# Kernel optimization log

Hardware: AMD Instinct MI355X
Metric: run time of the kernel (lower is better)

The kernel has to match this reference:

```python
import jax, jax.numpy as jnp
import numpy as np

B, L, D, H = 16, 1024, 1024, 16
HD = D // H  # head dim = 64


def setup_inputs() -> dict:
    rng = jax.random.key(0)
    ks = jax.random.split(rng, 12)
    s = 0.02
    return {
        "key": jax.random.normal(ks[0], (B, L, D), jnp.float32),
        "value": jax.random.normal(ks[1], (B, L, D), jnp.float32),
        "query": jax.random.normal(ks[2], (B, L, D), jnp.float32),
        "atten_masks": jax.random.randint(ks[3], (B, L, L), 0, 2, jnp.int32),
        "Wk": jax.random.normal(ks[4], (D, D), jnp.float32) * s,
        "bk": jnp.zeros((D,), jnp.float32),
        "Wq": jax.random.normal(ks[5], (D, D), jnp.float32) * s,
        "bq": jnp.zeros((D,), jnp.float32),
        "Wv": jax.random.normal(ks[6], (D, D), jnp.float32) * s,
        "bv": jnp.zeros((D,), jnp.float32),
        "Wp": jax.random.normal(ks[7], (D, D), jnp.float32) * s,
        "bp": jnp.zeros((D,), jnp.float32),
    }


def reference(key, value, query, atten_masks, Wk, bk, Wq, bq, Wv, bv, Wp, bp):
    # Linear projections (torch nn.Linear: x @ W^T + b)
    def lin(x, W, b):
        return x @ W.T + b

    # [B, L, D] -> [B, H, L, HD]
    def heads(x):
        return x.reshape(B, L, H, HD).transpose(0, 2, 1, 3)

    k = heads(lin(key, Wk, bk))
    q = heads(lin(query, Wq, bq))
    v = heads(lin(value, Wv, bv))

    scale = 1.0 / np.sqrt(HD).astype(np.float32)
    att = jnp.einsum("bhqd,bhkd->bhqk", q, k) * scale  # [B, H, L, L]
    att = jnp.where(atten_masks[:, None, :, :] == 0, -jnp.inf, att)
    att = jax.nn.softmax(att, axis=-1)

    y = jnp.einsum("bhqk,bhkd->bhqd", att, v)  # [B, H, L, HD]
    y = y.transpose(0, 2, 1, 3).reshape(B, L, D)
    return lin(y, Wp, bp)
```

## Files before the change

kernel.cpp:

```cpp
#include <hip/hip_runtime.h>

typedef __bf16 bf16_t;
typedef __bf16 bf16x4 __attribute__((ext_vector_type(4)));
typedef __bf16 bf16x8 __attribute__((ext_vector_type(8)));
typedef float f32x4 __attribute__((ext_vector_type(4)));
typedef float f32x16 __attribute__((ext_vector_type(16)));
typedef unsigned u32x2 __attribute__((ext_vector_type(2)));

__device__ __forceinline__ int swz(int row) { return (row ^ (row >> 3)) & 7; }
__device__ __forceinline__ int swz2(int row) { return (row ^ (row >> 2)) & 3; }

__device__ __forceinline__ f32x4 mfma16(bf16x8 a, bf16x8 b, f32x4 c) {
  return __builtin_amdgcn_mfma_f32_16x16x32_bf16(a, b, c, 0, 0, 0);
}
__device__ __forceinline__ f32x16 mfma32(bf16x8 a, bf16x8 b, f32x16 c) {
  return __builtin_amdgcn_mfma_f32_32x32x16_bf16(a, b, c, 0, 0, 0);
}

__device__ __forceinline__ void gl_lds16(const void* g, void* l) {
  __builtin_amdgcn_global_load_lds(
      (const __attribute__((address_space(1))) unsigned int*)g,
      (__attribute__((address_space(3))) unsigned int*)l, 16, 0, 0);
}

__global__ __launch_bounds__(256) void cvt_all_kernel(
    const float* __restrict__ key, const float* __restrict__ query,
    const float* __restrict__ value, const float* __restrict__ Wk,
    const float* __restrict__ Wq, const float* __restrict__ Wv,
    const float* __restrict__ Wp, const int* __restrict__ mask,
    bf16_t* __restrict__ I1, bf16_t* __restrict__ I2, bf16_t* __restrict__ I3,
    bf16_t* __restrict__ Wkb, bf16_t* __restrict__ Wqb,
    bf16_t* __restrict__ Wvb, bf16_t* __restrict__ Wpb,
    unsigned* __restrict__ mbits) {
  const int bid = blockIdx.x;
  if (bid >= 53248) {
    int idx = (bid - 53248) * 256 + threadIdx.x;
    const int4* src = (const int4*)(mask + (size_t)idx * 32);
    unsigned w = 0;
#pragma unroll
    for (int i = 0; i < 8; ++i) {
      int4 v = src[i];
      w |= (v.x != 0 ? 1u : 0u) << (i * 4 + 0);
      w |= (v.y != 0 ? 1u : 0u) << (i * 4 + 1);
      w |= (v.z != 0 ? 1u : 0u) << (i * 4 + 2);
      w |= (v.w != 0 ? 1u : 0u) << (i * 4 + 3);
    }
    mbits[idx] = w;
    return;
  }
  const float* s;
  bf16_t* d;
  int base;
  if (bid < 16384) { s = key; d = I1; base = bid; }
  else if (bid < 32768) { s = query; d = I2; base = bid - 16384; }
  else if (bid < 49152) { s = value; d = I3; base = bid - 32768; }
  else if (bid < 50176) { s = Wk; d = Wkb; base = bid - 49152; }
  else if (bid < 51200) { s = Wq; d = Wqb; base = bid - 50176; }
  else if (bid < 52224) { s = Wv; d = Wvb; base = bid - 51200; }
  else { s = Wp; d = Wpb; base = bid - 52224; }
  int i = base * 256 + threadIdx.x;
  float4 v = ((const float4*)s)[i];
  bf16x4 o;
  o[0] = (bf16_t)v.x; o[1] = (bf16_t)v.y; o[2] = (bf16_t)v.z; o[3] = (bf16_t)v.w;
  ((bf16x4*)d)[i] = o;
}

template <typename OT>
__device__ __forceinline__ void gemm256_body(const bf16_t* __restrict__ A,
                                             const bf16_t* __restrict__ W,
                                             const float* __restrict__ bias,
                                             OT* __restrict__ O) {
  extern __shared__ __align__(16) char smem[];
  bf16_t* AsBase = (bf16_t*)smem;
  bf16_t* BsBase = (bf16_t*)(smem + 3 * 8192 * 2);

  const int t = threadIdx.x;
  const int lane = t & 63;
  const int wid = t >> 6;
  const int g = lane >> 4;
  const int lr = lane & 15;
  const int wm = wid >> 2, wn = wid & 3;
  const int lid = blockIdx.x;
  const int logical = (lid & 7) * 32 + (lid >> 3);
  const int m0 = (logical >> 2) * 256;
  const int n0 = (logical & 3) * 256;

  f32x4 acc[8][4] = {};

  auto STAGE = [&](int buf, int kb) {
    bf16_t* Ab = AsBase + buf * 8192;
    bf16_t* Bb = BsBase + buf * 8192;
#pragma unroll
    for (int rr = 0; rr < 2; ++rr) {
      int s = rr * 512 + t;
      int row = s >> 2, c = s & 3;
      gl_lds16(A + (size_t)(m0 + row) * 1024 + kb + (c ^ swz2(row)) * 8,
               &Ab[(rr * 512 + wid * 64) * 8]);
      gl_lds16(W + (size_t)(n0 + row) * 1024 + kb + (c ^ swz2(row)) * 8,
               &Bb[(rr * 512 + wid * 64) * 8]);
    }
  };

  STAGE(0, 0);
  STAGE(1, 32);

  int cur = 0;
  for (int kb = 0; kb < 1024; kb += 32) {
    if (kb + 32 < 1024)
      asm volatile("s_waitcnt vmcnt(4)" ::: "memory");
    else
      asm volatile("s_waitcnt vmcnt(0)" ::: "memory");
    __builtin_amdgcn_sched_barrier(0);
    __builtin_amdgcn_s_barrier();
    __builtin_amdgcn_sched_barrier(0);

    if (kb + 64 < 1024) {
      int fut = cur + 2;
      if (fut >= 3) fut -= 3;
      STAGE(fut, kb + 64);
    }

    const bf16_t* Ab = AsBase + cur * 8192;
    const bf16_t* Bb = BsBase + cur * 8192;
    bf16x8 a[8], b[4];
#pragma unroll
    for (int i = 0; i < 8; ++i) {
      int row = wm * 128 + i * 16 + lr;
      a[i] = *(const bf16x8*)&Ab[row * 32 + ((g ^ swz2(row))) * 8];
    }
#pragma unroll
    for (int j = 0; j < 4; ++j) {
      int row = wn * 64 + j * 16 + lr;
      b[j] = *(const bf16x8*)&Bb[row * 32 + ((g ^ swz2(row))) * 8];
    }
    __builtin_amdgcn_s_setprio(1);
#pragma unroll
    for (int i = 0; i < 8; ++i)
#pragma unroll
      for (int j = 0; j < 4; ++j)
        acc[i][j] = mfma16(a[i], b[j], acc[i][j]);
    __builtin_amdgcn_s_setprio(0);

    cur = (cur == 2) ? 0 : cur + 1;
  }

  float bval[4];
#pragma unroll
  for (int j = 0; j < 4; ++j) bval[j] = bias[n0 + wn * 64 + j * 16 + lr];
#pragma unroll
  for (int i = 0; i < 8; ++i)
#pragma unroll
    for (int r = 0; r < 4; ++r) {
      int row = m0 + wm * 128 + i * 16 + g * 4 + r;
#pragma unroll
      for (int j = 0; j < 4; ++j) {
        int n = n0 + wn * 64 + j * 16 + lr;
        O[(size_t)row * 1024 + n] = (OT)(acc[i][j][r] + bval[j]);
      }
    }
}

__global__ __launch_bounds__(512, 2) void gemm256_qkv_kernel(
    const bf16_t* key, const bf16_t* query, const bf16_t* value,
    const bf16_t* Wkb, const bf16_t* Wqb, const bf16_t* Wvb, const float* bk,
    const float* bq, const float* bv, bf16_t* ko, bf16_t* qo, bf16_t* vo) {
  const bf16_t *A, *W;
  const float* bi;
  bf16_t* O;
  if (blockIdx.y == 0) { A = key; W = Wkb; bi = bk; O = ko; }
  else if (blockIdx.y == 1) { A = query; W = Wqb; bi = bq; O = qo; }
  else { A = value; W = Wvb; bi = bv; O = vo; }
  gemm256_body<bf16_t>(A, W, bi, O);
}

__global__ __launch_bounds__(512, 2) void gemm256_out_kernel(
    const bf16_t* __restrict__ A, const bf16_t* __restrict__ W,
    const float* __restrict__ b, float* __restrict__ O) {
  gemm256_body<float>(A, W, b, O);
}

__global__ __launch_bounds__(256) void transpose_v_kernel(
    const bf16_t* __restrict__ v_ws, bf16_t* __restrict__ vT) {
  __shared__ bf16_t T[64 * 66];
  const int kc = blockIdx.x, h = blockIdx.y, b = blockIdx.z;
  const int t = threadIdx.x;
  {
    int key = t >> 2, dblk = t & 3;
    const bf16_t* src =
        v_ws + ((size_t)(b * 1024 + kc * 64 + key)) * 1024 + h * 64 + dblk * 16;
    bf16x8 a0 = *(const bf16x8*)src;
    bf16x8 a1 = *(const bf16x8*)(src + 8);
    bf16_t* row = &T[key * 66 + dblk * 16];
#pragma unroll
    for (int j = 0; j < 4; ++j) {
      ((unsigned*)row)[j] = ((const unsigned*)&a0)[j];
      ((unsigned*)row)[j + 4] = ((const unsigned*)&a1)[j];
    }
  }
  __syncthreads();
  {
    int d = t >> 2, kcl = t & 3;
    bf16x8 o0, o1;
#pragma unroll
    for (int e = 0; e < 8; ++e) {
      o0[e] = T[(kcl * 16 + e) * 66 + d];
      o1[e] = T[(kcl * 16 + 8 + e) * 66 + d];
    }
    bf16_t* dst =
        vT + ((size_t)((b * 16 + h) * 64 + d)) * 1024 + kc * 64 + kcl * 16;
    *(bf16x8*)dst = o0;
    *(bf16x8*)(dst + 8) = o1;
  }
}

__global__ __launch_bounds__(256) void attn_kernel(
    const bf16_t* __restrict__ q_ws, const bf16_t* __restrict__ k_ws,
    const bf16_t* __restrict__ vT, const unsigned* __restrict__ mbits,
    bf16_t* __restrict__ y_ws) {
  __shared__ __align__(16) bf16_t Ks[64 * 64];
  __shared__ __align__(16) bf16_t Vs[64 * 64];

  const int lid = blockIdx.x;
  const int logical = (lid & 7) * 256 + (lid >> 3);
  const int qb = logical & 7;
  const int h = (logical >> 3) & 15;
  const int b = logical >> 7;
  const int t = threadIdx.x, lane = t & 63, wid = t >> 6;
  const int ql = lane & 31;
  const int hh = lane >> 5;
  const int q = qb * 128 + wid * 32 + ql;

  bf16x8 qf[4];
  {
    const bf16_t* qp = q_ws + ((size_t)(b * 1024 + q)) * 1024 + h * 64 + hh * 8;
#pragma unroll
    for (int kc = 0; kc < 4; ++kc) {
      bf16x8 raw = *(const bf16x8*)(qp + kc * 16);
      bf16x8 sc;
#pragma unroll
      for (int e = 0; e < 8; ++e)
        sc[e] = (bf16_t)((float)raw[e] * 0.18033688f);
      qf[kc] = sc;
    }
  }

  bf16x8 onesf;
#pragma unroll
  for (int e = 0; e < 8; ++e) onesf[e] = (bf16_t)1.0f;

  f32x16 acc0 = {}, acc1 = {}, accl = {};
  const bf16_t* Kb = k_ws + ((size_t)b * 1024) * 1024 + h * 64;
  const bf16_t* Vb = vT + ((size_t)((b * 16 + h) * 64)) * 1024;
  const unsigned* mrow = mbits + ((size_t)(b * 1024 + q)) * 32;

  for (int kb = 0; kb < 16; ++kb) {
    __syncthreads();
#pragma unroll
    for (int rr = 0; rr < 2; ++rr) {
      int s = rr * 256 + t;
      int row = s >> 3, c = s & 7;
      gl_lds16(Kb + (size_t)(kb * 64 + row) * 1024 + (c ^ swz(row)) * 8,
               &Ks[(rr * 256 + wid * 64) * 8]);
      gl_lds16(Vb + (size_t)row * 1024 + kb * 64 + (c ^ swz(row)) * 8,
               &Vs[(rr * 256 + wid * 64) * 8]);
    }
    uint2 mw = *(const uint2*)&mrow[kb * 2];
    __syncthreads();

    f32x16 c0 = {}, c1 = {};
    __builtin_amdgcn_s_setprio(1);
#pragma unroll
    for (int kc = 0; kc < 4; ++kc) {
      int sl = kc * 2 + hh;
      {
        int row = ql;
        bf16x8 kf = *(const bf16x8*)&Ks[row * 64 + ((sl ^ swz(row))) * 8];
        c0 = mfma32(kf, qf[kc], c0);
      }
      {
        int row = 32 + ql;
        bf16x8 kf = *(const bf16x8*)&Ks[row * 64 + ((sl ^ swz(row))) * 8];
        c1 = mfma32(kf, qf[kc], c1);
      }
    }
    __builtin_amdgcn_s_setprio(0);

    unsigned wx = mw.x >> (4 * hh);
    unsigned wy = mw.y >> (4 * hh);
    float p0[16], p1[16];
#pragma unroll
    for (int r = 0; r < 16; ++r) {
      const int posr = (r & 3) + 8 * (r >> 2);
      int n0m = (int)(wx << (31 - posr)) >> 31;
      int n1m = (int)(wy << (31 - posr)) >> 31;
      float e0 = __builtin_amdgcn_exp2f(c0[r]);
      float e1 = __builtin_amdgcn_exp2f(c1[r]);
      p0[r] = __int_as_float(__float_as_int(e0) & n0m);
      p1[r] = __int_as_float(__float_as_int(e1) & n1m);
    }

    bf16x8 pb[4];
#pragma unroll
    for (int kc = 0; kc < 4; ++kc) {
      const int base = (kc & 1) * 8;
      unsigned lo0, lo1, hi0, hi1;
      if (kc < 2) {
        union { bf16_t h[2]; unsigned u; } a0, a1, b0, b1;
        a0.h[0] = (bf16_t)p0[base + 0]; a0.h[1] = (bf16_t)p0[base + 1];
        a1.h[0] = (bf16_t)p0[base + 2]; a1.h[1] = (bf16_t)p0[base + 3];
        b0.h[0] = (bf16_t)p0[base + 4]; b0.h[1] = (bf16_t)p0[base + 5];
        b1.h[0] = (bf16_t)p0[base + 6]; b1.h[1] = (bf16_t)p0[base + 7];
        lo0 = a0.u; lo1 = a1.u; hi0 = b0.u; hi1 = b1.u;
      } else {
        union { bf16_t h[2]; unsigned u; } a0, a1, b0, b1;
        a0.h[0] = (bf16_t)p1[base + 0]; a0.h[1] = (bf16_t)p1[base + 1];
        a1.h[0] = (bf16_t)p1[base + 2]; a1.h[1] = (bf16_t)p1[base + 3];
        b0.h[0] = (bf16_t)p1[base + 4]; b0.h[1] = (bf16_t)p1[base + 5];
        b1.h[0] = (bf16_t)p1[base + 6]; b1.h[1] = (bf16_t)p1[base + 7];
        lo0 = a0.u; lo1 = a1.u; hi0 = b0.u; hi1 = b1.u;
      }
      u32x2 s0 = __builtin_amdgcn_permlane32_swap(lo0, hi0, false, false);
      u32x2 s1 = __builtin_amdgcn_permlane32_swap(lo1, hi1, false, false);
      union { unsigned u[4]; bf16x8 v; } pk;
      pk.u[0] = s0.x;
      pk.u[1] = s1.x;
      pk.u[2] = s0.y;
      pk.u[3] = s1.y;
      pb[kc] = pk.v;
    }

    __builtin_amdgcn_s_setprio(1);
#pragma unroll
    for (int kc = 0; kc < 4; ++kc) {
      int sl = kc * 2 + hh;
      {
        int row = ql;
        bf16x8 vf = *(const bf16x8*)&Vs[row * 64 + ((sl ^ swz(row))) * 8];
        acc0 = mfma32(vf, pb[kc], acc0);
      }
      {
        int row = 32 + ql;
        bf16x8 vf = *(const bf16x8*)&Vs[row * 64 + ((sl ^ swz(row))) * 8];
        acc1 = mfma32(vf, pb[kc], acc1);
      }
      accl = mfma32(onesf, pb[kc], accl);
    }
    __builtin_amdgcn_s_setprio(0);
  }

  float inv = 1.0f / fmaxf(accl[0], 1e-30f);
  bf16_t* yp = y_ws + ((size_t)(b * 1024 + q)) * 1024 + h * 64;
#pragma unroll
  for (int j = 0; j < 4; ++j) {
    bf16x4 o0, o1;
#pragma unroll
    for (int e = 0; e < 4; ++e) {
      o0[e] = (bf16_t)(acc0[4 * j + e] * inv);
      o1[e] = (bf16_t)(acc1[4 * j + e] * inv);
    }
    *(bf16x4*)&yp[8 * j + 4 * hh] = o0;
    *(bf16x4*)&yp[32 + 8 * j + 4 * hh] = o1;
  }
}

extern "C" void kernel_launch(void* const* d_in, const int* in_sizes, int n_in,
                              void* d_out, int out_size, void* d_ws,
                              size_t ws_size, hipStream_t stream) {
  (void)in_sizes; (void)n_in; (void)out_size; (void)ws_size;
  const float* key = (const float*)d_in[0];
  const float* value = (const float*)d_in[1];
  const float* query = (const float*)d_in[2];
  const int* mask = (const int*)d_in[3];
  const float* Wk = (const float*)d_in[4];
  const float* bk = (const float*)d_in[5];
  const float* Wq = (const float*)d_in[6];
  const float* bq = (const float*)d_in[7];
  const float* Wv = (const float*)d_in[8];
  const float* bv = (const float*)d_in[9];
  const float* Wp = (const float*)d_in[10];
  const float* bp = (const float*)d_in[11];
  float* out = (float*)d_out;

  char* ws = (char*)d_ws;
  const size_t MB = 1ull << 20;
  unsigned* mbits = (unsigned*)(ws);
  bf16_t* Wkb = (bf16_t*)(ws + 2 * MB);
  bf16_t* Wqb = (bf16_t*)(ws + 4 * MB);
  bf16_t* Wvb = (bf16_t*)(ws + 6 * MB);
  bf16_t* Wpb = (bf16_t*)(ws + 8 * MB);
  bf16_t* I1 = (bf16_t*)(ws + 10 * MB);
  bf16_t* I2 = (bf16_t*)(ws + 42 * MB);
  bf16_t* I3 = (bf16_t*)(ws + 74 * MB);
  bf16_t* k_ws = (bf16_t*)(ws + 106 * MB);
  bf16_t* q_ws = (bf16_t*)(ws + 138 * MB);
  bf16_t* v_ws = (bf16_t*)(ws + 170 * MB);
  bf16_t* vT_ws = I1;
  bf16_t* y_ws = I2;

  const size_t GEMM_LDS = 3 * 8192 * 2 * 2;

  cvt_all_kernel<<<55296, 256, 0, stream>>>(key, query, value, Wk, Wq, Wv, Wp,
                                            mask, I1, I2, I3, Wkb, Wqb, Wvb,
                                            Wpb, mbits);
  gemm256_qkv_kernel<<<dim3(256, 3), 512, GEMM_LDS, stream>>>(
      I1, I2, I3, Wkb, Wqb, Wvb, bk, bq, bv, k_ws, q_ws, v_ws);
  transpose_v_kernel<<<dim3(16, 16, 16), 256, 0, stream>>>(v_ws, vT_ws);
  attn_kernel<<<2048, 256, 0, stream>>>(q_ws, k_ws, vT_ws, mbits, y_ws);
  gemm256_out_kernel<<<256, 512, GEMM_LDS, stream>>>(y_ws, Wpb, bp, out);
}
```

Before: 355.2 us.

## Triple-buffer K/V tiles in attention and fold query scale into Wq

The attention kernel now keeps three LDS buffers for K and V tiles and prefetches tile kb+2 with global_load_lds while computing tile kb. This replaces the two barriers per iteration with a single barrier plus a manual vmcnt wait. The query scale factor, which includes log2e for exp2, moves from the attention kernel into the Wq conversion and the q bias. This saves per-element conversion work in attention at the cost of scaling Wq before its bf16 rounding, which changes rounding slightly. The hard-coded vmcnt(5) count depends on exactly how many vector memory ops are in flight, which is fragile.

Result: no change. 360.1 us (+1.4%).

```diff
diff --git a/kernel.cpp b/kernel.cpp
--- a/kernel.cpp
+++ b/kernel.cpp
@@ -6,6 +6,8 @@
 typedef float f32x4 __attribute__((ext_vector_type(4)));
 typedef float f32x16 __attribute__((ext_vector_type(16)));
 typedef unsigned u32x2 __attribute__((ext_vector_type(2)));
+
+#define QSCALE 0.18033688f
 
 __device__ __forceinline__ int swz(int row) { return (row ^ (row >> 3)) & 7; }
 __device__ __forceinline__ int swz2(int row) { return (row ^ (row >> 2)) & 3; }
@@ -51,17 +53,19 @@
   const float* s;
   bf16_t* d;
   int base;
+  float sc = 1.0f;
   if (bid < 16384) { s = key; d = I1; base = bid; }
   else if (bid < 32768) { s = query; d = I2; base = bid - 16384; }
   else if (bid < 49152) { s = value; d = I3; base = bid - 32768; }
   else if (bid < 50176) { s = Wk; d = Wkb; base = bid - 49152; }
-  else if (bid < 51200) { s = Wq; d = Wqb; base = bid - 50176; }
+  else if (bid < 51200) { s = Wq; d = Wqb; base = bid - 50176; sc = QSCALE; }
   else if (bid < 52224) { s = Wv; d = Wvb; base = bid - 51200; }
   else { s = Wp; d = Wpb; base = bid - 52224; }
   int i = base * 256 + threadIdx.x;
   float4 v = ((const float4*)s)[i];
   bf16x4 o;
-  o[0] = (bf16_t)v.x; o[1] = (bf16_t)v.y; o[2] = (bf16_t)v.z; o[3] = (bf16_t)v.w;
+  o[0] = (bf16_t)(v.x * sc); o[1] = (bf16_t)(v.y * sc);
+  o[2] = (bf16_t)(v.z * sc); o[3] = (bf16_t)(v.w * sc);
   ((bf16x4*)d)[i] = o;
 }
 
@@ -69,6 +73,7 @@
 __device__ __forceinline__ void gemm256_body(const bf16_t* __restrict__ A,
                                              const bf16_t* __restrict__ W,
                                              const float* __restrict__ bias,
+                                             float bscale,
                                              OT* __restrict__ O) {
   extern __shared__ __align__(16) char smem[];
   bf16_t* AsBase = (bf16_t*)smem;
@@ -146,7 +151,8 @@
 
   float bval[4];
 #pragma unroll
-  for (int j = 0; j < 4; ++j) bval[j] = bias[n0 + wn * 64 + j * 16 + lr];
+  for (int j = 0; j < 4; ++j)
+    bval[j] = bias[n0 + wn * 64 + j * 16 + lr] * bscale;
 #pragma unroll
   for (int i = 0; i < 8; ++i)
 #pragma unroll
@@ -167,16 +173,17 @@
   const bf16_t *A, *W;
   const float* bi;
   bf16_t* O;
+  float bs = 1.0f;
   if (blockIdx.y == 0) { A = key; W = Wkb; bi = bk; O = ko; }
-  else if (blockIdx.y == 1) { A = query; W = Wqb; bi = bq; O = qo; }
+  else if (blockIdx.y == 1) { A = query; W = Wqb; bi = bq; O = qo; bs = QSCALE; }
   else { A = value; W = Wvb; bi = bv; O = vo; }
-  gemm256_body<bf16_t>(A, W, bi, O);
+  gemm256_body<bf16_t>(A, W, bi, bs, O);
 }
 
 __global__ __launch_bounds__(512, 2) void gemm256_out_kernel(
     const bf16_t* __restrict__ A, const bf16_t* __restrict__ W,
     const float* __restrict__ b, float* __restrict__ O) {
-  gemm256_body<float>(A, W, b, O);
+  gemm256_body<float>(A, W, b, 1.0f, O);
 }
 
 __global__ __launch_bounds__(256) void transpose_v_kernel(
@@ -217,8 +224,8 @@
     const bf16_t* __restrict__ q_ws, const bf16_t* __restrict__ k_ws,
     const bf16_t* __restrict__ vT, const unsigned* __restrict__ mbits,
     bf16_t* __restrict__ y_ws) {
-  __shared__ __align__(16) bf16_t Ks[64 * 64];
-  __shared__ __align__(16) bf16_t Vs[64 * 64];
+  __shared__ __align__(16) bf16_t KsR[3][64 * 64];
+  __shared__ __align__(16) bf16_t VsR[3][64 * 64];
 
   const int lid = blockIdx.x;
   const int logical = (lid & 7) * 256 + (lid >> 3);
@@ -230,18 +237,27 @@
   const int hh = lane >> 5;
   const int q = qb * 128 + wid * 32 + ql;
 
+  const bf16_t* Kb = k_ws + ((size_t)b * 1024) * 1024 + h * 64;
+  const bf16_t* Vb = vT + ((size_t)((b * 16 + h) * 64)) * 1024;
+  const unsigned* mrow = mbits + ((size_t)(b * 1024 + q)) * 32;
+
+  auto STAGE = [&](int buf, int tile) {
+#pragma unroll
+    for (int rr = 0; rr < 2; ++rr) {
+      int s = rr * 256 + t;
+      int row = s >> 3, c = s & 7;
+      gl_lds16(Kb + (size_t)(tile * 64 + row) * 1024 + (c ^ swz(row)) * 8,
+               &KsR[buf][(rr * 256 + wid * 64) * 8]);
+      gl_lds16(Vb + (size_t)row * 1024 + tile * 64 + (c ^ swz(row)) * 8,
+               &VsR[buf][(rr * 256 + wid * 64) * 8]);
+    }
+  };
+
   bf16x8 qf[4];
   {
     const bf16_t* qp = q_ws + ((size_t)(b * 1024 + q)) * 1024 + h * 64 + hh * 8;
 #pragma unroll
-    for (int kc = 0; kc < 4; ++kc) {
-      bf16x8 raw = *(const bf16x8*)(qp + kc * 16);
-      bf16x8 sc;
-#pragma unroll
-      for (int e = 0; e < 8; ++e)
-        sc[e] = (bf16_t)((float)raw[e] * 0.18033688f);
-      qf[kc] = sc;
-    }
+    for (int kc = 0; kc < 4; ++kc) qf[kc] = *(const bf16x8*)(qp + kc * 16);
   }
 
   bf16x8 onesf;
@@ -249,23 +265,32 @@
   for (int e = 0; e < 8; ++e) onesf[e] = (bf16_t)1.0f;
 
   f32x16 acc0 = {}, acc1 = {}, accl = {};
-  const bf16_t* Kb = k_ws + ((size_t)b * 1024) * 1024 + h * 64;
-  const bf16_t* Vb = vT + ((size_t)((b * 16 + h) * 64)) * 1024;
-  const unsigned* mrow = mbits + ((size_t)(b * 1024 + q)) * 32;
-
+
+  uint2 mw_c = *(const uint2*)&mrow[0];
+  STAGE(0, 0);
+  uint2 mw_n = *(const uint2*)&mrow[2];
+  STAGE(1, 1);
+  uint2 mw_f = {0, 0};
+
+  int cur = 0;
   for (int kb = 0; kb < 16; ++kb) {
-    __syncthreads();
-#pragma unroll
-    for (int rr = 0; rr < 2; ++rr) {
-      int s = rr * 256 + t;
-      int row = s >> 3, c = s & 7;
-      gl_lds16(Kb + (size_t)(kb * 64 + row) * 1024 + (c ^ swz(row)) * 8,
-               &Ks[(rr * 256 + wid * 64) * 8]);
-      gl_lds16(Vb + (size_t)row * 1024 + kb * 64 + (c ^ swz(row)) * 8,
-               &Vs[(rr * 256 + wid * 64) * 8]);
-    }
-    uint2 mw = *(const uint2*)&mrow[kb * 2];
-    __syncthreads();
+    if (kb + 1 < 16)
+      asm volatile("s_waitcnt vmcnt(5)" ::: "memory");
+    else
+      asm volatile("s_waitcnt vmcnt(0)" ::: "memory");
+    __builtin_amdgcn_sched_barrier(0);
+    __builtin_amdgcn_s_barrier();
+    __builtin_amdgcn_sched_barrier(0);
+
+    if (kb + 2 < 16) {
+      int fut = cur + 2;
+      if (fut >= 3) fut -= 3;
+      mw_f = *(const uint2*)&mrow[(kb + 2) * 2];
+      STAGE(fut, kb + 2);
+    }
+
+    const bf16_t* Ks = KsR[cur];
+    const bf16_t* Vs = VsR[cur];
 
     f32x16 c0 = {}, c1 = {};
     __builtin_amdgcn_s_setprio(1);
@@ -285,8 +310,8 @@
     }
     __builtin_amdgcn_s_setprio(0);
 
-    unsigned wx = mw.x >> (4 * hh);
-    unsigned wy = mw.y >> (4 * hh);
+    unsigned wx = mw_c.x >> (4 * hh);
+    unsigned wy = mw_c.y >> (4 * hh);
     float p0[16], p1[16];
 #pragma unroll
     for (int r = 0; r < 16; ++r) {
@@ -346,6 +371,10 @@
       accl = mfma32(onesf, pb[kc], accl);
     }
     __builtin_amdgcn_s_setprio(0);
+
+    mw_c = mw_n;
+    mw_n = mw_f;
+    cur = (cur == 2) ? 0 : cur + 1;
   }
 
   float inv = 1.0f / fmaxf(accl[0], 1e-30f);
```

## Fold query scale into Wq conversion and process 128-key tiles per iteration

Applied to the files above, without the earlier changes.

The softmax scale (with its log2e factor) is folded into the bf16 conversion of Wq and into the q bias during the QKV GEMM epilogue, so the attention kernel loads Q fragments directly without per-element rescaling. The attention loop now stages 128 keys of K and V per iteration instead of 64, which halves the number of barrier-separated load phases. The inner computation is reorganized into four 32-key chunks that each do QK, masked exp2, pack, and PV. The cost is double the shared memory per block, which may reduce occupancy, and a slightly different bf16 rounding of the scaled Q weights.

After: 341.2 us. -3.9%, faster.

```diff
diff --git a/kernel.cpp b/kernel.cpp
--- a/kernel.cpp
+++ b/kernel.cpp
@@ -6,6 +6,8 @@
 typedef float f32x4 __attribute__((ext_vector_type(4)));
 typedef float f32x16 __attribute__((ext_vector_type(16)));
 typedef unsigned u32x2 __attribute__((ext_vector_type(2)));
+
+#define QSCALE 0.18033688f
 
 __device__ __forceinline__ int swz(int row) { return (row ^ (row >> 3)) & 7; }
 __device__ __forceinline__ int swz2(int row) { return (row ^ (row >> 2)) & 3; }
@@ -51,17 +53,19 @@
   const float* s;
   bf16_t* d;
   int base;
+  float sc = 1.0f;
   if (bid < 16384) { s = key; d = I1; base = bid; }
   else if (bid < 32768) { s = query; d = I2; base = bid - 16384; }
   else if (bid < 49152) { s = value; d = I3; base = bid - 32768; }
   else if (bid < 50176) { s = Wk; d = Wkb; base = bid - 49152; }
-  else if (bid < 51200) { s = Wq; d = Wqb; base = bid - 50176; }
+  else if (bid < 51200) { s = Wq; d = Wqb; base = bid - 50176; sc = QSCALE; }
   else if (bid < 52224) { s = Wv; d = Wvb; base = bid - 51200; }
   else { s = Wp; d = Wpb; base = bid - 52224; }
   int i = base * 256 + threadIdx.x;
   float4 v = ((const float4*)s)[i];
   bf16x4 o;
-  o[0] = (bf16_t)v.x; o[1] = (bf16_t)v.y; o[2] = (bf16_t)v.z; o[3] = (bf16_t)v.w;
+  o[0] = (bf16_t)(v.x * sc); o[1] = (bf16_t)(v.y * sc);
+  o[2] = (bf16_t)(v.z * sc); o[3] = (bf16_t)(v.w * sc);
   ((bf16x4*)d)[i] = o;
 }
 
@@ -69,6 +73,7 @@
 __device__ __forceinline__ void gemm256_body(const bf16_t* __restrict__ A,
                                              const bf16_t* __restrict__ W,
                                              const float* __restrict__ bias,
+                                             float bscale,
                                              OT* __restrict__ O) {
   extern __shared__ __align__(16) char smem[];
   bf16_t* AsBase = (bf16_t*)smem;
@@ -146,7 +151,8 @@
 
   float bval[4];
 #pragma unroll
-  for (int j = 0; j < 4; ++j) bval[j] = bias[n0 + wn * 64 + j * 16 + lr];
+  for (int j = 0; j < 4; ++j)
+    bval[j] = bias[n0 + wn * 64 + j * 16 + lr] * bscale;
 #pragma unroll
   for (int i = 0; i < 8; ++i)
 #pragma unroll
@@ -167,16 +173,17 @@
   const bf16_t *A, *W;
   const float* bi;
   bf16_t* O;
+  float bs = 1.0f;
   if (blockIdx.y == 0) { A = key; W = Wkb; bi = bk; O = ko; }
-  else if (blockIdx.y == 1) { A = query; W = Wqb; bi = bq; O = qo; }
+  else if (blockIdx.y == 1) { A = query; W = Wqb; bi = bq; O = qo; bs = QSCALE; }
   else { A = value; W = Wvb; bi = bv; O = vo; }
-  gemm256_body<bf16_t>(A, W, bi, O);
+  gemm256_body<bf16_t>(A, W, bi, bs, O);
 }
 
 __global__ __launch_bounds__(512, 2) void gemm256_out_kernel(
     const bf16_t* __restrict__ A, const bf16_t* __restrict__ W,
     const float* __restrict__ b, float* __restrict__ O) {
-  gemm256_body<float>(A, W, b, O);
+  gemm256_body<float>(A, W, b, 1.0f, O);
 }
 
 __global__ __launch_bounds__(256) void transpose_v_kernel(
@@ -217,8 +224,8 @@
     const bf16_t* __restrict__ q_ws, const bf16_t* __restrict__ k_ws,
     const bf16_t* __restrict__ vT, const unsigned* __restrict__ mbits,
     bf16_t* __restrict__ y_ws) {
-  __shared__ __align__(16) bf16_t Ks[64 * 64];
-  __shared__ __align__(16) bf16_t Vs[64 * 64];
+  __shared__ __align__(16) bf16_t Ks[128 * 64];
+  __shared__ __align__(16) bf16_t Vs[64 * 128];
 
   const int lid = blockIdx.x;
   const int logical = (lid & 7) * 256 + (lid >> 3);
@@ -234,14 +241,7 @@
   {
     const bf16_t* qp = q_ws + ((size_t)(b * 1024 + q)) * 1024 + h * 64 + hh * 8;
 #pragma unroll
-    for (int kc = 0; kc < 4; ++kc) {
-      bf16x8 raw = *(const bf16x8*)(qp + kc * 16);
-      bf16x8 sc;
-#pragma unroll
-      for (int e = 0; e < 8; ++e)
-        sc[e] = (bf16_t)((float)raw[e] * 0.18033688f);
-      qf[kc] = sc;
-    }
+    for (int kc = 0; kc < 4; ++kc) qf[kc] = *(const bf16x8*)(qp + kc * 16);
   }
 
   bf16x8 onesf;
@@ -253,99 +253,84 @@
   const bf16_t* Vb = vT + ((size_t)((b * 16 + h) * 64)) * 1024;
   const unsigned* mrow = mbits + ((size_t)(b * 1024 + q)) * 32;
 
-  for (int kb = 0; kb < 16; ++kb) {
+  for (int kb = 0; kb < 8; ++kb) {
     __syncthreads();
 #pragma unroll
-    for (int rr = 0; rr < 2; ++rr) {
+    for (int rr = 0; rr < 4; ++rr) {
       int s = rr * 256 + t;
       int row = s >> 3, c = s & 7;
-      gl_lds16(Kb + (size_t)(kb * 64 + row) * 1024 + (c ^ swz(row)) * 8,
+      gl_lds16(Kb + (size_t)(kb * 128 + row) * 1024 + (c ^ swz(row)) * 8,
                &Ks[(rr * 256 + wid * 64) * 8]);
-      gl_lds16(Vb + (size_t)row * 1024 + kb * 64 + (c ^ swz(row)) * 8,
+    }
+#pragma unroll
+    for (int rr = 0; rr < 4; ++rr) {
+      int s = rr * 256 + t;
+      int row = s >> 4, c = s & 15;
+      gl_lds16(Vb + (size_t)row * 1024 + kb * 128 + ((c ^ swz(row))) * 8,
                &Vs[(rr * 256 + wid * 64) * 8]);
     }
-    uint2 mw = *(const uint2*)&mrow[kb * 2];
+    uint4 mw = *(const uint4*)&mrow[kb * 4];
     __syncthreads();
 
-    f32x16 c0 = {}, c1 = {};
-    __builtin_amdgcn_s_setprio(1);
-#pragma unroll
-    for (int kc = 0; kc < 4; ++kc) {
-      int sl = kc * 2 + hh;
-      {
-        int row = ql;
-        bf16x8 kf = *(const bf16x8*)&Ks[row * 64 + ((sl ^ swz(row))) * 8];
-        c0 = mfma32(kf, qf[kc], c0);
-      }
-      {
-        int row = 32 + ql;
-        bf16x8 kf = *(const bf16x8*)&Ks[row * 64 + ((sl ^ swz(row))) * 8];
-        c1 = mfma32(kf, qf[kc], c1);
-      }
-    }
-    __builtin_amdgcn_s_setprio(0);
-
-    unsigned wx = mw.x >> (4 * hh);
-    unsigned wy = mw.y >> (4 * hh);
-    float p0[16], p1[16];
-#pragma unroll
-    for (int r = 0; r < 16; ++r) {
-      const int posr = (r & 3) + 8 * (r >> 2);
-      int n0m = (int)(wx << (31 - posr)) >> 31;
-      int n1m = (int)(wy << (31 - posr)) >> 31;
-      float e0 = __builtin_amdgcn_exp2f(c0[r]);
-      float e1 = __builtin_amdgcn_exp2f(c1[r]);
-      p0[r] = __int_as_float(__float_as_int(e0) & n0m);
-      p1[r] = __int_as_float(__float_as_int(e1) & n1m);
-    }
-
-    bf16x8 pb[4];
-#pragma unroll
-    for (int kc = 0; kc < 4; ++kc) {
-      const int base = (kc & 1) * 8;
-      unsigned lo0, lo1, hi0, hi1;
-      if (kc < 2) {
+#pragma unroll
+    for (int ct = 0; ct < 4; ++ct) {
+      f32x16 c = {};
+      __builtin_amdgcn_s_setprio(1);
+#pragma unroll
+      for (int kc = 0; kc < 4; ++kc) {
+        int row = ct * 32 + ql;
+        bf16x8 kf = *(const bf16x8*)&Ks[row * 64 + (((kc * 2 + hh) ^ swz(row))) * 8];
+        c = mfma32(kf, qf[kc], c);
+      }
+      __builtin_amdgcn_s_setprio(0);
+
+      unsigned w = ((const unsigned*)&mw)[ct] >> (4 * hh);
+      float p[16];
+#pragma unroll
+      for (int r = 0; r < 16; ++r) {
+        const int posr = (r & 3) + 8 * (r >> 2);
+        int nm = (int)(w << (31 - posr)) >> 31;
+        float e0 = __builtin_amdgcn_exp2f(c[r]);
+        p[r] = __int_as_float(__float_as_int(e0) & nm);
+      }
+
+      bf16x8 pbt[2];
+#pragma unroll
+      for (int j = 0; j < 2; ++j) {
+        const int base = j * 8;
         union { bf16_t h[2]; unsigned u; } a0, a1, b0, b1;
-        a0.h[0] = (bf16_t)p0[base + 0]; a0.h[1] = (bf16_t)p0[base + 1];
-        a1.h[0] = (bf16_t)p0[base + 2]; a1.h[1] = (bf16_t)p0[base + 3];
-        b0.h[0] = (bf16_t)p0[base + 4]; b0.h[1] = (bf16_t)p0[base + 5];
-        b1.h[0] = (bf16_t)p0[base + 6]; b1.h[1] = (bf16_t)p0[base + 7];
-        lo0 = a0.u; lo1 = a1.u; hi0 = b0.u; hi1 = b1.u;
-      } else {
-        union { bf16_t h[2]; unsigned u; } a0, a1, b0, b1;
-        a0.h[0] = (bf16_t)p1[base + 0]; a0.h[1] = (bf16_t)p1[base + 1];
-        a1.h[0] = (bf16_t)p1[base + 2]; a1.h[1] = (bf16_t)p1[base + 3];
-        b0.h[0] = (bf16_t)p1[base + 4]; b0.h[1] = (bf16_t)p1[base + 5];
-        b1.h[0] = (bf16_t)p1[base + 6]; b1.h[1] = (bf16_t)p1[base + 7];
-        lo0 = a0.u; lo1 = a1.u; hi0 = b0.u; hi1 = b1.u;
-      }
-      u32x2 s0 = __builtin_amdgcn_permlane32_swap(lo0, hi0, false, false);
-      u32x2 s1 = __builtin_amdgcn_permlane32_swap(lo1, hi1, false, false);
-      union { unsigned u[4]; bf16x8 v; } pk;
-      pk.u[0] = s0.x;
-      pk.u[1] = s1.x;
-      pk.u[2] = s0.y;
-      pk.u[3] = s1.y;
-      pb[kc] = pk.v;
-    }
-
-    __builtin_amdgcn_s_setprio(1);
-#pragma unroll
-    for (int kc = 0; kc < 4; ++kc) {
-      int sl = kc * 2 + hh;
-      {
-        int row = ql;
-        bf16x8 vf = *(const bf16x8*)&Vs[row * 64 + ((sl ^ swz(row))) * 8];
-        acc0 = mfma32(vf, pb[kc], acc0);
-      }
-      {
-        int row = 32 + ql;
-        bf16x8 vf = *(const bf16x8*)&Vs[row * 64 + ((sl ^ swz(row))) * 8];
-        acc1 = mfma32(vf, pb[kc], acc1);
-      }
-      accl = mfma32(onesf, pb[kc], accl);
-    }
-    __builtin_amdgcn_s_setprio(0);
+        a0.h[0] = (bf16_t)p[base + 0]; a0.h[1] = (bf16_t)p[base + 1];
+        a1.h[0] = (bf16_t)p[base + 2]; a1.h[1] = (bf16_t)p[base + 3];
+        b0.h[0] = (bf16_t)p[base + 4]; b0.h[1] = (bf16_t)p[base + 5];
+        b1.h[0] = (bf16_t)p[base + 6]; b1.h[1] = (bf16_t)p[base + 7];
+        u32x2 s0 = __builtin_amdgcn_permlane32_swap(a0.u, b0.u, false, false);
+        u32x2 s1 = __builtin_amdgcn_permlane32_swap(a1.u, b1.u, false, false);
+        union { unsigned u[4]; bf16x8 v; } pk;
+        pk.u[0] = s0.x;
+        pk.u[1] = s1.x;
+        pk.u[2] = s0.y;
+        pk.u[3] = s1.y;
+        pbt[j] = pk.v;
+      }
+
+      __builtin_amdgcn_s_setprio(1);
+#pragma unroll
+      for (int j = 0; j < 2; ++j) {
+        int sl = (2 * ct + j) * 2 + hh;
+        {
+          int row = ql;
+          bf16x8 vf = *(const bf16x8*)&Vs[row * 128 + ((sl ^ swz(row))) * 8];
+          acc0 = mfma32(vf, pbt[j], acc0);
+        }
+        {
+          int row = 32 + ql;
+          bf16x8 vf = *(const bf16x8*)&Vs[row * 128 + ((sl ^ swz(row))) * 8];
+          acc1 = mfma32(vf, pbt[j], acc1);
+        }
+        accl = mfma32(onesf, pbt[j], accl);
+      }
+      __builtin_amdgcn_s_setprio(0);
+    }
   }
 
   float inv = 1.0f / fmaxf(accl[0], 1e-30f);
```
